# Kernel tuning notes

Measured on AMD Instinct MI355X. Metric: run time of the kernel, lower is better.

Reference implementation:

```python
import jax, jax.numpy as jnp
import numpy as np

D_MODEL = 1024
NUM_HEAD = 16
HEAD_DIM = D_MODEL // NUM_HEAD
D_OUT = 1024
B, S = 2, 2048


def setup_inputs() -> dict:
    key = jax.random.key(0)
    ks = jax.random.split(key, 11)
    s = 0.02
    return {
        "Q": jax.random.normal(ks[0], (B, S, D_MODEL), jnp.float32),
        "K": jax.random.normal(ks[1], (B, S, D_MODEL), jnp.float32),
        "V": jax.random.normal(ks[2], (B, S, D_MODEL), jnp.float32),
        "Wq": jax.random.normal(ks[3], (D_MODEL, D_MODEL), jnp.float32) * s,
        "bq": jnp.zeros((D_MODEL,), jnp.float32),
        "Wk": jax.random.normal(ks[4], (D_MODEL, D_MODEL), jnp.float32) * s,
        "bk": jnp.zeros((D_MODEL,), jnp.float32),
        "Wv": jax.random.normal(ks[5], (D_MODEL, D_MODEL), jnp.float32) * s,
        "bv": jnp.zeros((D_MODEL,), jnp.float32),
        "Wo": jax.random.normal(ks[6], (D_MODEL, D_OUT), jnp.float32) * s,
        "bo": jnp.zeros((D_OUT,), jnp.float32),
    }


def reference(Q, K, V, Wq, bq, Wk, bk, Wv, bv, Wo, bo):
    T = jnp.asarray(HEAD_DIM, Q.dtype) ** 0.5
    b = Q.shape[0]
    q = (Q @ Wq + bq) / T                      # [B,S,D]
    k = K @ Wk + bk
    v = V @ Wv + bv
    q = q.reshape(b, -1, NUM_HEAD, HEAD_DIM)   # [B,S,H,d]
    k = k.reshape(b, -1, NUM_HEAD, HEAD_DIM)
    v = v.reshape(b, -1, NUM_HEAD, HEAD_DIM)
    scores = jnp.einsum("bqhd,bkhd->bhqk", q, k)
    attn = jax.nn.softmax(scores, axis=-1)
    out = jnp.einsum("bhqk,bkhd->bqhd", attn, v).reshape(b, -1, D_MODEL)
    return out @ Wo + bo
```

## Files before the change

kernel.cpp:

```cpp
#include <hip/hip_runtime.h>
#include <cstdint>
#include <cstddef>

#define D_MODEL 1024
#define HD 64
#define NH 16
#define SEQ 2048
#define NB 2

typedef __attribute__((ext_vector_type(8))) short bf8;
typedef __attribute__((ext_vector_type(8))) unsigned short us8;
typedef __attribute__((ext_vector_type(4))) unsigned short us4;
typedef __attribute__((ext_vector_type(4))) float f4;

__device__ __forceinline__ float bf2f(unsigned short u) {
  union { unsigned int i; float f; } c; c.i = ((unsigned int)u) << 16; return c.f;
}
__device__ __forceinline__ unsigned short f2bf(float x) {
  union { float f; unsigned int i; } c; c.f = x;
  unsigned int r = (c.i + 0x7FFFu + ((c.i >> 16) & 1u)) >> 16;
  return (unsigned short)r;
}
__device__ __forceinline__ unsigned int pkbf(float lo, float hi) {
  unsigned int r;
  asm("v_cvt_pk_bf16_f32 %0, %1, %2" : "=v"(r) : "v"(lo), "v"(hi));
  return r;
}
__device__ __forceinline__ float ex2(float x) {
  float r;
  asm("v_exp_f32 %0, %1" : "=v"(r) : "v"(x));
  return r;
}
__device__ __forceinline__ f4 mfma16(bf8 a, bf8 b, f4 c) {
  return __builtin_amdgcn_mfma_f32_16x16x32_bf16(a, b, c, 0, 0, 0);
}
__device__ __forceinline__ void gl16(const unsigned short* g, unsigned short* l) {
  __builtin_amdgcn_global_load_lds(
      (const __attribute__((address_space(1))) unsigned int*)g,
      (__attribute__((address_space(3))) unsigned int*)l, 16, 0, 0);
}

#define QSCALE (0.125f * 1.44269504088896f)

__global__ __launch_bounds__(256) void prep_all(
    const float* __restrict__ Q, const float* __restrict__ K, const float* __restrict__ V,
    const float* __restrict__ Wq, const float* __restrict__ Wk,
    const float* __restrict__ Wv, const float* __restrict__ Wo,
    unsigned short* __restrict__ dq, unsigned short* __restrict__ dk,
    unsigned short* __restrict__ dv,
    unsigned short* __restrict__ wthi, unsigned short* __restrict__ wtlo) {
  int bid = blockIdx.x;
  __shared__ float ls[32][33];
  if (bid < 6144) {
    int z = bid >> 11, x = bid & 2047;
    const float* s = (z == 0) ? Q : (z == 1) ? K : V;
    unsigned short* d = (z == 0) ? dq : (z == 1) ? dk : dv;
    size_t i = ((size_t)x * 256 + threadIdx.x) * 8;
    float4 a = *reinterpret_cast<const float4*>(s + i);
    float4 b = *reinterpret_cast<const float4*>(s + i + 4);
    union { us8 v; unsigned int u[4]; } o;
    o.u[0] = pkbf(a.x, a.y); o.u[1] = pkbf(a.z, a.w);
    o.u[2] = pkbf(b.x, b.y); o.u[3] = pkbf(b.z, b.w);
    *reinterpret_cast<us8*>(d + i) = o.v;
  } else {
    int j = bid - 6144;
    int mat = j >> 10, rem = j & 1023;
    int kt = (rem >> 5) * 32, nt = (rem & 31) * 32;
    const float* W = (mat == 0) ? Wq : (mat == 1) ? Wk : (mat == 2) ? Wv : Wo;
    unsigned short* oh = wthi + ((size_t)mat << 20);
    unsigned short* ol = wtlo + ((size_t)mat << 20);
    int i = threadIdx.x >> 5;
    int jj = threadIdx.x & 31;
#pragma unroll
    for (int ii = 0; ii < 4; ++ii) {
      int r = i + ii * 8;
      ls[r][jj] = W[(size_t)(kt + r) * D_MODEL + nt + jj];
    }
    __syncthreads();
#pragma unroll
    for (int ii = 0; ii < 4; ++ii) {
      int r = i + ii * 8;
      float v = ls[jj][r];
      if (mat == 0) v *= QSCALE;
      unsigned short h = f2bf(v);
      size_t o = (size_t)(nt + r) * D_MODEL + kt + jj;
      oh[o] = h;
      if (mat == 3) ol[o] = f2bf(v - bf2f(h));
    }
  }
}

__global__ __launch_bounds__(256, 3) void gemm_kernel(
    const unsigned short* __restrict__ A0, const unsigned short* __restrict__ A1,
    const unsigned short* __restrict__ A2, const unsigned short* __restrict__ wth,
    const float* __restrict__ b0, const float* __restrict__ b1,
    const float* __restrict__ b2,
    unsigned short* __restrict__ qh, unsigned short* __restrict__ kh,
    unsigned short* __restrict__ vt) {
  int z = blockIdx.z;
  const unsigned short* A = (z == 0) ? A0 : (z == 1) ? A1 : A2;
  const unsigned short* Bh = wth + ((size_t)z << 20);
  const float* bias = (z == 0) ? b0 : (z == 1) ? b1 : b2;
  float bsc = (z == 0) ? QSCALE : 1.0f;

  int bm = blockIdx.y, bn = blockIdx.x;
  int tid = threadIdx.x, lane = tid & 63, w = tid >> 6;
  int wr = w >> 1, wc = w & 1, l16 = lane & 15, l4 = lane >> 4;

  __shared__ unsigned short As[2][128 * 32];
  __shared__ unsigned short Bsh[2][128 * 32];

  const unsigned short* Ab = A + (size_t)(bm * 128) * D_MODEL;
  const unsigned short* Bhb = Bh + (size_t)(bn * 128) * D_MODEL;

  int r0 = tid >> 2, g0 = tid & 3;
  int r1 = (256 + tid) >> 2, g1 = tid & 3;
  int s0 = (r0 ^ (r0 >> 2)) & 3, s1 = (r1 ^ (r1 >> 2)) & 3;
  size_t so0 = (size_t)r0 * D_MODEL + ((g0 ^ s0) * 8);
  size_t so1 = (size_t)r1 * D_MODEL + ((g1 ^ s1) * 8);
  int ld0 = (w * 64) * 8;
  int ld1 = (256 + w * 64) * 8;

  int offA[4], offB[4];
#pragma unroll
  for (int m = 0; m < 4; ++m) {
    int row = wr * 64 + m * 16 + l16;
    int sw = (row ^ (row >> 2)) & 3;
    offA[m] = row * 32 + ((l4 ^ sw)) * 8;
  }
#pragma unroll
  for (int n = 0; n < 4; ++n) {
    int row = wc * 64 + n * 16 + l16;
    int sw = (row ^ (row >> 2)) & 3;
    offB[n] = row * 32 + ((l4 ^ sw)) * 8;
  }

  f4 acc[4][4];
  const f4 zf = {0.f, 0.f, 0.f, 0.f};
#pragma unroll
  for (int m = 0; m < 4; ++m)
#pragma unroll
    for (int n = 0; n < 4; ++n) acc[m][n] = zf;

  gl16(Ab + so0, &As[0][ld0]);  gl16(Ab + so1, &As[0][ld1]);
  gl16(Bhb + so0, &Bsh[0][ld0]); gl16(Bhb + so1, &Bsh[0][ld1]);
  __syncthreads();

  int cur = 0;
  for (int i = 0; i < 32; ++i) {
    if (i < 31) {
      int ktn = (i + 1) * 32;
      gl16(Ab + ktn + so0, &As[cur ^ 1][ld0]);  gl16(Ab + ktn + so1, &As[cur ^ 1][ld1]);
      gl16(Bhb + ktn + so0, &Bsh[cur ^ 1][ld0]); gl16(Bhb + ktn + so1, &Bsh[cur ^ 1][ld1]);
    }
    bf8 a[4], bh[4];
#pragma unroll
    for (int m = 0; m < 4; ++m)
      a[m] = *reinterpret_cast<const bf8*>(&As[cur][offA[m]]);
#pragma unroll
    for (int n = 0; n < 4; ++n)
      bh[n] = *reinterpret_cast<const bf8*>(&Bsh[cur][offB[n]]);
#pragma unroll
    for (int m = 0; m < 4; ++m)
#pragma unroll
      for (int n = 0; n < 4; ++n)
        acc[m][n] = mfma16(a[m], bh[n], acc[m][n]);
    __syncthreads();
    cur ^= 1;
  }

#pragma unroll
  for (int n = 0; n < 4; ++n) {
    int col = bn * 128 + wc * 64 + n * 16 + l16;
    float bb = bias[col] * bsc;
#pragma unroll
    for (int m = 0; m < 4; ++m) {
      int row0 = bm * 128 + wr * 64 + m * 16 + l4 * 4;
      if (z == 0) {
#pragma unroll
        for (int r = 0; r < 4; ++r)
          qh[(size_t)(row0 + r) * D_MODEL + col] = f2bf(acc[m][n][r] + bb);
      } else if (z == 1) {
#pragma unroll
        for (int r = 0; r < 4; ++r)
          kh[(size_t)(row0 + r) * D_MODEL + col] = f2bf(acc[m][n][r] + bb);
      } else {
        int bb2 = row0 >> 11, ss = row0 & (SEQ - 1);
        int hh2 = col >> 6, dd = col & 63;
        union { us4 s; uint2 u; } pk4;
        pk4.u.x = pkbf(acc[m][n][0] + bb, acc[m][n][1] + bb);
        pk4.u.y = pkbf(acc[m][n][2] + bb, acc[m][n][3] + bb);
        *reinterpret_cast<us4*>(vt + ((size_t)(bb2 * NH + hh2) * HD + dd) * SEQ + ss) = pk4.s;
      }
    }
  }
}

__global__ __launch_bounds__(256, 3) void out_gemm(
    const unsigned short* __restrict__ ah, const unsigned short* __restrict__ wth,
    const unsigned short* __restrict__ wtl, const float* __restrict__ bo,
    float* __restrict__ o32) {
  const unsigned short* Bh = wth + ((size_t)3 << 20);
  const unsigned short* Bl = wtl + ((size_t)3 << 20);
  int bm = blockIdx.y, bn = blockIdx.x;
  int tid = threadIdx.x, lane = tid & 63, w = tid >> 6;
  int wr = w >> 1, wc = w & 1, l16 = lane & 15, l4 = lane >> 4;

  __shared__ unsigned short As[2][128 * 32];
  __shared__ unsigned short Bsh[2][64 * 32];
  __shared__ unsigned short Bsl[2][64 * 32];

  const unsigned short* Ab = ah + (size_t)(bm * 128) * D_MODEL;
  const unsigned short* Bhb = Bh + (size_t)(bn * 64) * D_MODEL;
  const unsigned short* Blb = Bl + (size_t)(bn * 64) * D_MODEL;

  int r0 = tid >> 2, g0 = tid & 3;
  int r1 = (256 + tid) >> 2;
  int s0 = (r0 ^ (r0 >> 2)) & 3, s1 = (r1 ^ (r1 >> 2)) & 3;
  size_t so0 = (size_t)r0 * D_MODEL + ((g0 ^ s0) * 8);
  size_t so1 = (size_t)r1 * D_MODEL + ((g0 ^ s1) * 8);
  int ld0 = (w * 64) * 8;
  int ld1 = (256 + w * 64) * 8;

  int offA[4], offB[2];
#pragma unroll
  for (int m = 0; m < 4; ++m) {
    int row = wr * 64 + m * 16 + l16;
    int sw = (row ^ (row >> 2)) & 3;
    offA[m] = row * 32 + ((l4 ^ sw)) * 8;
  }
#pragma unroll
  for (int n = 0; n < 2; ++n) {
    int row = wc * 32 + n * 16 + l16;
    int sw = (row ^ (row >> 2)) & 3;
    offB[n] = row * 32 + ((l4 ^ sw)) * 8;
  }

  f4 acc[4][2];
  const f4 zf = {0.f, 0.f, 0.f, 0.f};
#pragma unroll
  for (int m = 0; m < 4; ++m)
#pragma unroll
    for (int n = 0; n < 2; ++n) acc[m][n] = zf;

  gl16(Ab + so0, &As[0][ld0]); gl16(Ab + so1, &As[0][ld1]);
  gl16(Bhb + so0, &Bsh[0][ld0]);
  gl16(Blb + so0, &Bsl[0][ld0]);
  __syncthreads();

  int cur = 0;
  for (int i = 0; i < 32; ++i) {
    if (i < 31) {
      int ktn = (i + 1) * 32;
      gl16(Ab + ktn + so0, &As[cur ^ 1][ld0]); gl16(Ab + ktn + so1, &As[cur ^ 1][ld1]);
      gl16(Bhb + ktn + so0, &Bsh[cur ^ 1][ld0]);
      gl16(Blb + ktn + so0, &Bsl[cur ^ 1][ld0]);
    }
    bf8 a[4], bh[2], bl[2];
#pragma unroll
    for (int m = 0; m < 4; ++m)
      a[m] = *reinterpret_cast<const bf8*>(&As[cur][offA[m]]);
#pragma unroll
    for (int n = 0; n < 2; ++n) {
      bh[n] = *reinterpret_cast<const bf8*>(&Bsh[cur][offB[n]]);
      bl[n] = *reinterpret_cast<const bf8*>(&Bsl[cur][offB[n]]);
    }
#pragma unroll
    for (int m = 0; m < 4; ++m)
#pragma unroll
      for (int n = 0; n < 2; ++n) {
        acc[m][n] = mfma16(a[m], bh[n], acc[m][n]);
        acc[m][n] = mfma16(a[m], bl[n], acc[m][n]);
      }
    __syncthreads();
    cur ^= 1;
  }

#pragma unroll
  for (int n = 0; n < 2; ++n) {
    int col = bn * 64 + wc * 32 + n * 16 + l16;
    float bb = bo[col];
#pragma unroll
    for (int m = 0; m < 4; ++m) {
      int row0 = bm * 128 + wr * 64 + m * 16 + l4 * 4;
#pragma unroll
      for (int r = 0; r < 4; ++r)
        o32[(size_t)(row0 + r) * D_MODEL + col] = acc[m][n][r] + bb;
    }
  }
}

__global__ __launch_bounds__(256) void attn_kernel(
    const unsigned short* __restrict__ qh, const unsigned short* __restrict__ kh,
    const unsigned short* __restrict__ vt, unsigned short* __restrict__ aout) {
  int orig = blockIdx.x + (blockIdx.y << 4) + (blockIdx.z << 8);
  int swz = ((orig & 7) << 6) + (orig >> 3);
  int qt = swz & 15, h = (swz >> 4) & 15, b = swz >> 8;

  int tid = threadIdx.x;
  int lane = tid & 63, w = tid >> 6;
  int l16 = lane & 15, l4 = lane >> 4;
  int l8r = lane >> 3, l8c = lane & 7;

  __shared__ unsigned short lds[32768];

  const unsigned short* Kh = kh + (size_t)b * SEQ * D_MODEL + h * HD;
  const unsigned short* Vt = vt + (size_t)(b * NH + h) * HD * SEQ;

  bf8 qf[2][2];
#pragma unroll
  for (int m = 0; m < 2; ++m) {
    size_t qo = (size_t)(b * SEQ + qt * 128 + w * 32 + m * 16 + l16) * D_MODEL + h * HD + l4 * 8;
    qf[m][0] = *reinterpret_cast<const bf8*>(qh + qo);
    qf[m][1] = *reinterpret_cast<const bf8*>(qh + qo + 32);
  }
  bf8 ones;
#pragma unroll
  for (int j = 0; j < 8; ++j) ones[j] = (short)0x3F80;

  const f4 zf = {0.f, 0.f, 0.f, 0.f};
  f4 acc[2][4];
  f4 accs[2] = {zf, zf};
  float mr[2] = {0.f, 0.f};
#pragma unroll
  for (int m = 0; m < 2; ++m)
#pragma unroll
    for (int nt = 0; nt < 4; ++nt) acc[m][nt] = zf;

  const int sgr = (l8c ^ l8r) * 8;
  const int swk = l16 & 7;
  const int vsub = ((l4 & 1) << 2);
  const int vrow_in = lane >> 4;

  {
#pragma unroll
    for (int j = 0; j < 4; ++j) {
      int s = w * 4 + j;
      gl16(Kh + (size_t)(8 * s + l8r) * D_MODEL + sgr, &lds[0 + s * 512]);
      int row = 4 * s + vrow_in;
      int g = ((lane & 7) ^ (row & 7)) | (lane & 8);
      gl16(Vt + (size_t)row * SEQ + g * 8, &lds[16384 + s * 512]);
    }
  }
  __syncthreads();

  int cur = 0;
  for (int kt = 0; kt < SEQ / 128; ++kt) {
    if (kt < SEQ / 128 - 1) {
      int k0n = (kt + 1) * 128;
      unsigned short* kd = &lds[(cur ^ 1) * 8192];
      unsigned short* vd = &lds[16384 + (cur ^ 1) * 8192];
#pragma unroll
      for (int j = 0; j < 4; ++j) {
        int s = w * 4 + j;
        gl16(Kh + (size_t)(k0n + 8 * s + l8r) * D_MODEL + sgr, kd + s * 512);
        int row = 4 * s + vrow_in;
        int g = ((lane & 7) ^ (row & 7)) | (lane & 8);
        gl16(Vt + (size_t)row * SEQ + k0n + g * 8, vd + s * 512);
      }
    }
    const unsigned short* khb = &lds[cur * 8192];
    const unsigned short* vlb = &lds[16384 + cur * 8192];

#pragma unroll
    for (int h2 = 0; h2 < 2; ++h2) {
      const unsigned short* khh = khb + h2 * 4096;
      bf8 kb[4][2];
#pragma unroll
      for (int c = 0; c < 4; ++c) {
        int row = c * 16 + l16;
        kb[c][0] = *reinterpret_cast<const bf8*>(&khh[row * 64 + ((l4 ^ swk) * 8)]);
        kb[c][1] = *reinterpret_cast<const bf8*>(&khh[row * 64 + (((4 + l4) ^ swk) * 8)]);
      }
      f4 sc[2][4];
      __builtin_amdgcn_s_setprio(1);
#pragma unroll
      for (int m = 0; m < 2; ++m)
#pragma unroll
        for (int c = 0; c < 4; ++c) {
          f4 sv = zf;
          sv = mfma16(kb[c][0], qf[m][0], sv);
          sv = mfma16(kb[c][1], qf[m][1], sv);
          sc[m][c] = sv;
        }
      __builtin_amdgcn_s_setprio(0);
      uint2 vdr[4][4];
#pragma unroll
      for (int c = 0; c < 4; ++c) {
        int gvc = 2 * c + (l4 >> 1);
        int voff = (((gvc ^ swk) + 8 * h2) << 3) + vsub;
#pragma unroll
        for (int nt = 0; nt < 4; ++nt)
          vdr[c][nt] = *reinterpret_cast<const uint2*>(&vlb[(nt * 16 + l16) * 128 + voff]);
      }
      unsigned Wp[2][4][2];
#pragma unroll
      for (int m = 0; m < 2; ++m) {
        float tc0 = fmaxf(fmaxf(sc[m][0][0], sc[m][0][1]), fmaxf(sc[m][0][2], sc[m][0][3]));
        float tc1 = fmaxf(fmaxf(sc[m][1][0], sc[m][1][1]), fmaxf(sc[m][1][2], sc[m][1][3]));
        float tc2 = fmaxf(fmaxf(sc[m][2][0], sc[m][2][1]), fmaxf(sc[m][2][2], sc[m][2][3]));
        float tc3 = fmaxf(fmaxf(sc[m][3][0], sc[m][3][1]), fmaxf(sc[m][3][2], sc[m][3][3]));
        float tm = fmaxf(fmaxf(tc0, tc1), fmaxf(tc2, tc3));
        tm = fmaxf(tm, __shfl_xor(tm, 16));
        tm = fmaxf(tm, __shfl_xor(tm, 32));
        if (__any(tm > mr[m] + 8.0f)) {
          float mn = fmaxf(mr[m], tm);
          float al = ex2(mr[m] - mn);
          mr[m] = mn;
          accs[m][0] *= al; accs[m][1] *= al; accs[m][2] *= al; accs[m][3] *= al;
#pragma unroll
          for (int nt = 0; nt < 4; ++nt) {
            acc[m][nt][0] *= al; acc[m][nt][1] *= al;
            acc[m][nt][2] *= al; acc[m][nt][3] *= al;
          }
        }
#pragma unroll
        for (int c = 0; c < 4; ++c) {
          float p0 = ex2(sc[m][c][0] - mr[m]);
          float p1 = ex2(sc[m][c][1] - mr[m]);
          float p2 = ex2(sc[m][c][2] - mr[m]);
          float p3 = ex2(sc[m][c][3] - mr[m]);
          Wp[m][c][0] = pkbf(p0, p1);
          Wp[m][c][1] = pkbf(p2, p3);
        }
      }
      __builtin_amdgcn_s_setprio(1);
#pragma unroll
      for (int cp = 0; cp < 2; ++cp) {
        int c0 = cp * 2, c1 = cp * 2 + 1;
#pragma unroll
        for (int m = 0; m < 2; ++m) {
          union { bf8 v; unsigned u[4]; } pu;
          pu.u[0] = Wp[m][c0][0]; pu.u[1] = Wp[m][c0][1];
          pu.u[2] = Wp[m][c1][0]; pu.u[3] = Wp[m][c1][1];
          accs[m] = mfma16(ones, pu.v, accs[m]);
#pragma unroll
          for (int nt = 0; nt < 4; ++nt) {
            union { bf8 v; unsigned u[4]; } vu;
            vu.u[0] = vdr[c0][nt].x; vu.u[1] = vdr[c0][nt].y;
            vu.u[2] = vdr[c1][nt].x; vu.u[3] = vdr[c1][nt].y;
            acc[m][nt] = mfma16(vu.v, pu.v, acc[m][nt]);
          }
        }
      }
      __builtin_amdgcn_s_setprio(0);
    }
    __syncthreads();
    cur ^= 1;
  }

  float inv[2];
#pragma unroll
  for (int m = 0; m < 2; ++m) inv[m] = 1.0f / accs[m][0];
#pragma unroll
  for (int m = 0; m < 2; ++m) {
    int q = w * 32 + m * 16 + l16;
    int sw = (q & 7) << 3;
#pragma unroll
    for (int nt = 0; nt < 4; ++nt) {
      uint2 pw;
      pw.x = pkbf(acc[m][nt][0] * inv[m], acc[m][nt][1] * inv[m]);
      pw.y = pkbf(acc[m][nt][2] * inv[m], acc[m][nt][3] * inv[m]);
      int d0 = nt * 16 + l4 * 4;
      *reinterpret_cast<uint2*>(&lds[q * 64 + (d0 ^ sw)]) = pw;
    }
  }
  __syncthreads();
  {
    int q = tid >> 1, dh = (tid & 1) * 32, sw = (q & 7) << 3;
    size_t orow = ((size_t)(b * SEQ + qt * 128 + q)) * D_MODEL + h * HD + dh;
#pragma unroll
    for (int j = 0; j < 4; ++j) {
      us8 vv = *reinterpret_cast<const us8*>(&lds[q * 64 + ((dh + j * 8) ^ sw)]);
      *reinterpret_cast<us8*>(&aout[orow + j * 8]) = vv;
    }
  }
}

extern "C" void kernel_launch(void* const* d_in, const int* in_sizes, int n_in,
                              void* d_out, int out_size, void* d_ws, size_t ws_size,
                              hipStream_t stream) {
  const float* Q  = (const float*)d_in[0];
  const float* K  = (const float*)d_in[1];
  const float* V  = (const float*)d_in[2];
  const float* Wq = (const float*)d_in[3];
  const float* bq = (const float*)d_in[4];
  const float* Wk = (const float*)d_in[5];
  const float* bk = (const float*)d_in[6];
  const float* Wv = (const float*)d_in[7];
  const float* bv = (const float*)d_in[8];
  const float* Wo = (const float*)d_in[9];
  const float* bo = (const float*)d_in[10];
  float* out = (float*)d_out;

  unsigned char* ws = (unsigned char*)d_ws;
  const size_t MB = 1024 * 1024;
  unsigned short* wthi = (unsigned short*)(ws);
  unsigned short* wtlo = (unsigned short*)(ws + 8 * MB);
  unsigned short* qh   = (unsigned short*)(ws + 16 * MB);
  unsigned short* kh   = (unsigned short*)(ws + 24 * MB);
  unsigned short* vt   = (unsigned short*)(ws + 32 * MB);
  unsigned short* ah   = (unsigned short*)(ws + 40 * MB);
  unsigned short* vbf  = (unsigned short*)(ws + 48 * MB);
  unsigned short* qbf  = (unsigned short*)d_out;
  unsigned short* kbf  = (unsigned short*)d_out + 4 * MB;

  prep_all<<<dim3(10240, 1, 1), 256, 0, stream>>>(Q, K, V, Wq, Wk, Wv, Wo,
                                                  qbf, kbf, vbf, wthi, wtlo);
  gemm_kernel<<<dim3(8, 32, 3), 256, 0, stream>>>(qbf, kbf, vbf, wthi,
                                                  bq, bk, bv, qh, kh, vt);
  attn_kernel<<<dim3(16, NH, NB), 256, 0, stream>>>(qh, kh, vt, ah);
  out_gemm<<<dim3(16, 32, 1), 256, 0, stream>>>(ah, wthi, wtlo, bo, out);
}
```

Measured before the change: 142.3 us.

## Fuse activation bf16 conversion into projection GEMM and drop split-precision output weights

Removes the separate pass that converted Q/K/V activations to bf16. The projection GEMM now loads fp32 tiles into registers, converts them, and stores them to LDS while the MFMAs run. The out-projection also stops using the hi/lo bf16 split of Wo, which halves its MFMA count and weight traffic at the cost of accuracy. Register-staged A loads replace the async LDS loads, which may cost some latency hiding.

```diff
diff --git a/kernel.cpp b/kernel.cpp
--- a/kernel.cpp
+++ b/kernel.cpp
@@ -42,63 +42,42 @@
 
 #define QSCALE (0.125f * 1.44269504088896f)
 
-__global__ __launch_bounds__(256) void prep_all(
-    const float* __restrict__ Q, const float* __restrict__ K, const float* __restrict__ V,
+__global__ __launch_bounds__(256) void prep_weights(
     const float* __restrict__ Wq, const float* __restrict__ Wk,
     const float* __restrict__ Wv, const float* __restrict__ Wo,
-    unsigned short* __restrict__ dq, unsigned short* __restrict__ dk,
-    unsigned short* __restrict__ dv,
-    unsigned short* __restrict__ wthi, unsigned short* __restrict__ wtlo) {
+    unsigned short* __restrict__ wthi) {
   int bid = blockIdx.x;
+  int mat = bid >> 10, rem = bid & 1023;
+  int kt = (rem >> 5) * 32, nt = (rem & 31) * 32;
+  const float* W = (mat == 0) ? Wq : (mat == 1) ? Wk : (mat == 2) ? Wv : Wo;
+  unsigned short* oh = wthi + ((size_t)mat << 20);
   __shared__ float ls[32][33];
-  if (bid < 6144) {
-    int z = bid >> 11, x = bid & 2047;
-    const float* s = (z == 0) ? Q : (z == 1) ? K : V;
-    unsigned short* d = (z == 0) ? dq : (z == 1) ? dk : dv;
-    size_t i = ((size_t)x * 256 + threadIdx.x) * 8;
-    float4 a = *reinterpret_cast<const float4*>(s + i);
-    float4 b = *reinterpret_cast<const float4*>(s + i + 4);
-    union { us8 v; unsigned int u[4]; } o;
-    o.u[0] = pkbf(a.x, a.y); o.u[1] = pkbf(a.z, a.w);
-    o.u[2] = pkbf(b.x, b.y); o.u[3] = pkbf(b.z, b.w);
-    *reinterpret_cast<us8*>(d + i) = o.v;
-  } else {
-    int j = bid - 6144;
-    int mat = j >> 10, rem = j & 1023;
-    int kt = (rem >> 5) * 32, nt = (rem & 31) * 32;
-    const float* W = (mat == 0) ? Wq : (mat == 1) ? Wk : (mat == 2) ? Wv : Wo;
-    unsigned short* oh = wthi + ((size_t)mat << 20);
-    unsigned short* ol = wtlo + ((size_t)mat << 20);
-    int i = threadIdx.x >> 5;
-    int jj = threadIdx.x & 31;
-#pragma unroll
-    for (int ii = 0; ii < 4; ++ii) {
-      int r = i + ii * 8;
-      ls[r][jj] = W[(size_t)(kt + r) * D_MODEL + nt + jj];
-    }
-    __syncthreads();
-#pragma unroll
-    for (int ii = 0; ii < 4; ++ii) {
-      int r = i + ii * 8;
-      float v = ls[jj][r];
-      if (mat == 0) v *= QSCALE;
-      unsigned short h = f2bf(v);
-      size_t o = (size_t)(nt + r) * D_MODEL + kt + jj;
-      oh[o] = h;
-      if (mat == 3) ol[o] = f2bf(v - bf2f(h));
-    }
-  }
-}
-
-__global__ __launch_bounds__(256, 3) void gemm_kernel(
-    const unsigned short* __restrict__ A0, const unsigned short* __restrict__ A1,
-    const unsigned short* __restrict__ A2, const unsigned short* __restrict__ wth,
+  int i = threadIdx.x >> 5;
+  int jj = threadIdx.x & 31;
+#pragma unroll
+  for (int ii = 0; ii < 4; ++ii) {
+    int r = i + ii * 8;
+    ls[r][jj] = W[(size_t)(kt + r) * D_MODEL + nt + jj];
+  }
+  __syncthreads();
+#pragma unroll
+  for (int ii = 0; ii < 4; ++ii) {
+    int r = i + ii * 8;
+    float v = ls[jj][r];
+    if (mat == 0) v *= QSCALE;
+    oh[(size_t)(nt + r) * D_MODEL + kt + jj] = f2bf(v);
+  }
+}
+
+__global__ __launch_bounds__(256, 3) void proj_gemm(
+    const float* __restrict__ Qin, const float* __restrict__ Kin,
+    const float* __restrict__ Vin, const unsigned short* __restrict__ wth,
     const float* __restrict__ b0, const float* __restrict__ b1,
     const float* __restrict__ b2,
     unsigned short* __restrict__ qh, unsigned short* __restrict__ kh,
     unsigned short* __restrict__ vt) {
   int z = blockIdx.z;
-  const unsigned short* A = (z == 0) ? A0 : (z == 1) ? A1 : A2;
+  const float* A = (z == 0) ? Qin : (z == 1) ? Kin : Vin;
   const unsigned short* Bh = wth + ((size_t)z << 20);
   const float* bias = (z == 0) ? b0 : (z == 1) ? b1 : b2;
   float bsc = (z == 0) ? QSCALE : 1.0f;
@@ -110,7 +89,7 @@
   __shared__ unsigned short As[2][128 * 32];
   __shared__ unsigned short Bsh[2][128 * 32];
 
-  const unsigned short* Ab = A + (size_t)(bm * 128) * D_MODEL;
+  const float* Ab = A + (size_t)(bm * 128) * D_MODEL;
   const unsigned short* Bhb = Bh + (size_t)(bn * 128) * D_MODEL;
 
   int r0 = tid >> 2, g0 = tid & 3;
@@ -121,6 +100,15 @@
   int ld0 = (w * 64) * 8;
   int ld1 = (256 + w * 64) * 8;
 
+  int rr = tid >> 2, c8 = (tid & 3) * 8;
+  int adst[2];
+#pragma unroll
+  for (int p = 0; p < 2; ++p) {
+    int row = p * 64 + rr;
+    int sw = (row ^ (row >> 2)) & 3;
+    adst[p] = row * 32 + (((tid & 3) ^ sw)) * 8;
+  }
+
   int offA[4], offB[4];
 #pragma unroll
   for (int m = 0; m < 4; ++m) {
@@ -142,16 +130,39 @@
 #pragma unroll
     for (int n = 0; n < 4; ++n) acc[m][n] = zf;
 
-  gl16(Ab + so0, &As[0][ld0]);  gl16(Ab + so1, &As[0][ld1]);
-  gl16(Bhb + so0, &Bsh[0][ld0]); gl16(Bhb + so1, &Bsh[0][ld1]);
+  {
+    float4 x[2][2];
+#pragma unroll
+    for (int p = 0; p < 2; ++p) {
+      const float* src = Ab + (size_t)(p * 64 + rr) * D_MODEL + c8;
+      x[p][0] = *reinterpret_cast<const float4*>(src);
+      x[p][1] = *reinterpret_cast<const float4*>(src + 4);
+    }
+    gl16(Bhb + so0, &Bsh[0][ld0]);
+    gl16(Bhb + so1, &Bsh[0][ld1]);
+#pragma unroll
+    for (int p = 0; p < 2; ++p) {
+      union { us8 v; unsigned u[4]; } hv;
+      hv.u[0] = pkbf(x[p][0].x, x[p][0].y); hv.u[1] = pkbf(x[p][0].z, x[p][0].w);
+      hv.u[2] = pkbf(x[p][1].x, x[p][1].y); hv.u[3] = pkbf(x[p][1].z, x[p][1].w);
+      *reinterpret_cast<us8*>(&As[0][adst[p]]) = hv.v;
+    }
+  }
   __syncthreads();
 
   int cur = 0;
   for (int i = 0; i < 32; ++i) {
+    float4 nx[2][2];
     if (i < 31) {
       int ktn = (i + 1) * 32;
-      gl16(Ab + ktn + so0, &As[cur ^ 1][ld0]);  gl16(Ab + ktn + so1, &As[cur ^ 1][ld1]);
-      gl16(Bhb + ktn + so0, &Bsh[cur ^ 1][ld0]); gl16(Bhb + ktn + so1, &Bsh[cur ^ 1][ld1]);
+#pragma unroll
+      for (int p = 0; p < 2; ++p) {
+        const float* src = Ab + (size_t)(p * 64 + rr) * D_MODEL + ktn + c8;
+        nx[p][0] = *reinterpret_cast<const float4*>(src);
+        nx[p][1] = *reinterpret_cast<const float4*>(src + 4);
+      }
+      gl16(Bhb + ktn + so0, &Bsh[cur ^ 1][ld0]);
+      gl16(Bhb + ktn + so1, &Bsh[cur ^ 1][ld1]);
     }
     bf8 a[4], bh[4];
 #pragma unroll
@@ -165,6 +176,15 @@
 #pragma unroll
       for (int n = 0; n < 4; ++n)
         acc[m][n] = mfma16(a[m], bh[n], acc[m][n]);
+    if (i < 31) {
+#pragma unroll
+      for (int p = 0; p < 2; ++p) {
+        union { us8 v; unsigned u[4]; } hv;
+        hv.u[0] = pkbf(nx[p][0].x, nx[p][0].y); hv.u[1] = pkbf(nx[p][0].z, nx[p][0].w);
+        hv.u[2] = pkbf(nx[p][1].x, nx[p][1].y); hv.u[3] = pkbf(nx[p][1].z, nx[p][1].w);
+        *reinterpret_cast<us8*>(&As[cur ^ 1][adst[p]]) = hv.v;
+      }
+    }
     __syncthreads();
     cur ^= 1;
   }
@@ -198,21 +218,17 @@
 
 __global__ __launch_bounds__(256, 3) void out_gemm(
     const unsigned short* __restrict__ ah, const unsigned short* __restrict__ wth,
-    const unsigned short* __restrict__ wtl, const float* __restrict__ bo,
-    float* __restrict__ o32) {
+    const float* __restrict__ bo, float* __restrict__ o32) {
   const unsigned short* Bh = wth + ((size_t)3 << 20);
-  const unsigned short* Bl = wtl + ((size_t)3 << 20);
   int bm = blockIdx.y, bn = blockIdx.x;
   int tid = threadIdx.x, lane = tid & 63, w = tid >> 6;
   int wr = w >> 1, wc = w & 1, l16 = lane & 15, l4 = lane >> 4;
 
   __shared__ unsigned short As[2][128 * 32];
   __shared__ unsigned short Bsh[2][64 * 32];
-  __shared__ unsigned short Bsl[2][64 * 32];
 
   const unsigned short* Ab = ah + (size_t)(bm * 128) * D_MODEL;
   const unsigned short* Bhb = Bh + (size_t)(bn * 64) * D_MODEL;
-  const unsigned short* Blb = Bl + (size_t)(bn * 64) * D_MODEL;
 
   int r0 = tid >> 2, g0 = tid & 3;
   int r1 = (256 + tid) >> 2;
@@ -245,7 +261,6 @@
 
   gl16(Ab + so0, &As[0][ld0]); gl16(Ab + so1, &As[0][ld1]);
   gl16(Bhb + so0, &Bsh[0][ld0]);
-  gl16(Blb + so0, &Bsl[0][ld0]);
   __syncthreads();
 
   int cur = 0;
@@ -254,24 +269,19 @@
       int ktn = (i + 1) * 32;
       gl16(Ab + ktn + so0, &As[cur ^ 1][ld0]); gl16(Ab + ktn + so1, &As[cur ^ 1][ld1]);
       gl16(Bhb + ktn + so0, &Bsh[cur ^ 1][ld0]);
-      gl16(Blb + ktn + so0, &Bsl[cur ^ 1][ld0]);
-    }
-    bf8 a[4], bh[2], bl[2];
+    }
+    bf8 a[4], bh[2];
 #pragma unroll
     for (int m = 0; m < 4; ++m)
       a[m] = *reinterpret_cast<const bf8*>(&As[cur][offA[m]]);
 #pragma unroll
-    for (int n = 0; n < 2; ++n) {
+    for (int n = 0; n < 2; ++n)
       bh[n] = *reinterpret_cast<const bf8*>(&Bsh[cur][offB[n]]);
-      bl[n] = *reinterpret_cast<const bf8*>(&Bsl[cur][offB[n]]);
-    }
 #pragma unroll
     for (int m = 0; m < 4; ++m)
 #pragma unroll
-      for (int n = 0; n < 2; ++n) {
+      for (int n = 0; n < 2; ++n)
         acc[m][n] = mfma16(a[m], bh[n], acc[m][n]);
-        acc[m][n] = mfma16(a[m], bl[n], acc[m][n]);
-      }
     __syncthreads();
     cur ^= 1;
   }
@@ -496,19 +506,14 @@
   unsigned char* ws = (unsigned char*)d_ws;
   const size_t MB = 1024 * 1024;
   unsigned short* wthi = (unsigned short*)(ws);
-  unsigned short* wtlo = (unsigned short*)(ws + 8 * MB);
-  unsigned short* qh   = (unsigned short*)(ws + 16 * MB);
-  unsigned short* kh   = (unsigned short*)(ws + 24 * MB);
-  unsigned short* vt   = (unsigned short*)(ws + 32 * MB);
-  unsigned short* ah   = (unsigned short*)(ws + 40 * MB);
-  unsigned short* vbf  = (unsigned short*)(ws + 48 * MB);
-  unsigned short* qbf  = (unsigned short*)d_out;
-  unsigned short* kbf  = (unsigned short*)d_out + 4 * MB;
-
-  prep_all<<<dim3(10240, 1, 1), 256, 0, stream>>>(Q, K, V, Wq, Wk, Wv, Wo,
-                                                  qbf, kbf, vbf, wthi, wtlo);
-  gemm_kernel<<<dim3(8, 32, 3), 256, 0, stream>>>(qbf, kbf, vbf, wthi,
-                                                  bq, bk, bv, qh, kh, vt);
+  unsigned short* qh   = (unsigned short*)(ws + 8 * MB);
+  unsigned short* kh   = (unsigned short*)(ws + 16 * MB);
+  unsigned short* vt   = (unsigned short*)(ws + 24 * MB);
+  unsigned short* ah   = (unsigned short*)(ws + 32 * MB);
+
+  prep_weights<<<dim3(4096, 1, 1), 256, 0, stream>>>(Wq, Wk, Wv, Wo, wthi);
+  proj_gemm<<<dim3(8, 32, 3), 256, 0, stream>>>(Q, K, V, wthi,
+                                                bq, bk, bv, qh, kh, vt);
   attn_kernel<<<dim3(16, NH, NB), 256, 0, stream>>>(qh, kh, vt, ah);
-  out_gemm<<<dim3(16, 32, 1), 256, 0, stream>>>(ah, wthi, wtlo, bo, out);
-}
+  out_gemm<<<dim3(16, 32, 1), 256, 0, stream>>>(ah, wthi, bo, out);
+}
```

After: 148.3 us. 4.2% more time.
